# Performance work log

Hardware: AMD Instinct MI355X
Metric: run time of the kernel (lower is better)

## Reference

```python
import jax, jax.numpy as jnp
import numpy as np

BITS = 4
GROUP_SIZE = 128
IN_FEATURES = 4096
OUT_FEATURES = 11008
BATCH = 128


def setup_inputs() -> dict:
    key = jax.random.key(0)
    k1, k2, k3, k4 = jax.random.split(key, 4)
    x = jax.random.normal(k1, (BATCH, IN_FEATURES), dtype=jnp.float32)
    # packed 4-bit weights: each int32 holds 8 nibbles along the in-feature dim
    qweight = jax.random.randint(k2, (IN_FEATURES // 32 * BITS, OUT_FEATURES), 0, 2147483647, dtype=jnp.int32)
    n_groups = IN_FEATURES // GROUP_SIZE
    scales = jax.random.uniform(k3, (n_groups, OUT_FEATURES), dtype=jnp.float32) * 0.01 + 1e-3
    # note: in GPTQLinear_woo, `zeros` buffer already stores scale*zero_point
    zeros = jax.random.normal(k4, (n_groups, OUT_FEATURES), dtype=jnp.float32) * 0.01
    return {"x": x, "qweight": qweight, "scales": scales, "zeros": zeros}


def _dequant(qweight, scales, zeros):
    out_f = qweight.shape[1]
    shifts = jnp.arange(0, 32, BITS, dtype=jnp.int32)  # [8]
    # [in/8, 8, out] -> unpack nibbles (mask kills arithmetic-shift sign bits)
    w = (qweight[:, None, :] >> shifts[None, :, None]) & (2 ** BITS - 1)
    w = w.reshape(-1, GROUP_SIZE, out_f).astype(scales.dtype)  # [n_groups, gs, out]
    w = scales[:, None, :] * w - zeros[:, None, :]
    return w.reshape(-1, out_f)  # [in, out]


def reference(x, qweight, scales, zeros):
    w = _dequant(qweight, scales, zeros)
    return jnp.matmul(x, w)  # [batch, out]
```

## Files before the change

### kernel.cpp

```cpp
#include <hip/hip_runtime.h>
#include <hip/hip_bf16.h>
#include <stdint.h>


#define IN_F   4096
#define OUT_F  11008
#define BATCH  128
#define SPLIT  4
#define KSLICE (IN_F / SPLIT)
#define NCH    (KSLICE / 64)
#define NCHG   (IN_F / 64)
#define NBN    86
#define NBLK   (NBN * 2 * SPLIT)
#define MN     (BATCH * OUT_F)

typedef __attribute__((ext_vector_type(8)))  short short8;
typedef __attribute__((ext_vector_type(16))) float f32x16;

static __device__ __forceinline__ unsigned int f2bf_pack(float lo, float hi) {
  unsigned int a = __float_as_uint(lo);
  unsigned int b = __float_as_uint(hi);
  a += 0x7FFFu + ((a >> 16) & 1u);
  b += 0x7FFFu + ((b >> 16) & 1u);
  return (a >> 16) | (b & 0xFFFF0000u);
}

__global__ __launch_bounds__(256) void cvt_swz(const float* __restrict__ x,
                                               uint4* __restrict__ xs) {
  int t  = blockIdx.x * 256 + threadIdx.x;
  int m  = t >> 9;
  int k  = (t & 511) * 8;
  float4 u0 = *(const float4*)(x + (size_t)m * IN_F + k);
  float4 u1 = *(const float4*)(x + (size_t)m * IN_F + k + 4);
  uint4 o;
  o.x = f2bf_pack(u0.x, u0.y);
  o.y = f2bf_pack(u0.z, u0.w);
  o.z = f2bf_pack(u1.x, u1.y);
  o.w = f2bf_pack(u1.z, u1.w);
  int mt = m >> 5, lo32 = m & 31;
  int cg = k >> 6, ks = (k >> 4) & 3, hi = (k >> 3) & 1;
  size_t idx = (size_t)(((mt * NCHG + cg) * 4 + ks) << 6) + hi * 32 + lo32;
  xs[idx] = o;
}

__global__ __launch_bounds__(256) void zero_out(float* __restrict__ out) {
  int base = (blockIdx.x * 256 + threadIdx.x) * 16;
  float4 z = {0.f, 0.f, 0.f, 0.f};
#pragma unroll
  for (int j = 0; j < 4; ++j) *(float4*)(out + base + j * 4) = z;
}

__global__ __launch_bounds__(256) void reduce_kernel(const float* __restrict__ part,
                                                     float* __restrict__ out) {
  int base = (blockIdx.x * 256 + threadIdx.x) * 8;
  float4 s0 = {0.f, 0.f, 0.f, 0.f}, s1 = s0;
#pragma unroll
  for (int s = 0; s < SPLIT; ++s) {
    const float* p = part + (size_t)s * MN + base;
    float4 a = *(const float4*)(p);
    float4 b = *(const float4*)(p + 4);
    s0.x += a.x; s0.y += a.y; s0.z += a.z; s0.w += a.w;
    s1.x += b.x; s1.y += b.y; s1.z += b.z; s1.w += b.w;
  }
  *(float4*)(out + base)     = s0;
  *(float4*)(out + base + 4) = s1;
}

static __device__ __forceinline__ short8 deq8(unsigned int q, float s, float z) {
  float f[8];
#pragma unroll
  for (int j = 0; j < 8; ++j)
    f[j] = s * (float)((q >> (4 * j)) & 0xFu) - z;
  union { unsigned int u[4]; short8 s8; } r;
#pragma unroll
  for (int j = 0; j < 4; ++j)
    r.u[j] = f2bf_pack(f[2 * j], f[2 * j + 1]);
  return r.s8;
}

#define LOAD_Q(S, CC) do {                                                     \
    _Pragma("unroll")                                                          \
    for (int ks_ = 0; ks_ < 4; ++ks_)                                          \
      qP[S][ks_] = qlane[(size_t)((CC) * 8 + ks_ * 2) * OUT_F];                \
  } while (0)

__global__ __launch_bounds__(256) void gptq_gemm(
    const uint4* __restrict__ xs,
    const int* __restrict__ qweight,
    const float* __restrict__ scales,
    const float* __restrict__ zeros,
    float* __restrict__ outp,
    int atomic_mode) {
  const int tid  = threadIdx.x;
  const int lane = tid & 63;
  const int wid  = tid >> 6;
  const int hi   = lane >> 5;
  const int lo32 = lane & 31;

  const int nb = blockIdx.x % NBN;
  const int mb = (blockIdx.x / NBN) & 1;
  const int sl = blockIdx.x / (NBN * 2);

  const int ncol = nb * 128 + wid * 32 + lo32;
  const int m0   = mb * 64;

  float* dst = atomic_mode ? outp : outp + (size_t)sl * MN;

  float sreg[8], zreg[8];
#pragma unroll
  for (int g = 0; g < 8; ++g) {
    sreg[g] = scales[(size_t)(sl * 8 + g) * OUT_F + ncol];
    zreg[g] = zeros [(size_t)(sl * 8 + g) * OUT_F + ncol];
  }

  const int* qlane = qweight + (size_t)(sl * (KSLICE / 8) + hi) * OUT_F + ncol;
  const uint4* aB0 = xs + (size_t)(((mb * 2 + 0) * NCHG + sl * NCH) << 8) + lane;
  const uint4* aB1 = xs + (size_t)(((mb * 2 + 1) * NCHG + sl * NCH) << 8) + lane;

  unsigned int qP[3][4];
  LOAD_Q(0, 0);
  LOAD_Q(1, 1);
  LOAD_Q(2, 2);

  f32x16 acc[2] = {};

#pragma unroll
  for (int cc = 0; cc < NCH; ++cc) {
    uint4 aF[2][4];
#pragma unroll
    for (int ks = 0; ks < 4; ++ks) {
      aF[0][ks] = aB0[(size_t)(cc * 4 + ks) << 6];
      aF[1][ks] = aB1[(size_t)(cc * 4 + ks) << 6];
    }

    const float s = sreg[cc >> 1], z = zreg[cc >> 1];
    short8 bF[4];
#pragma unroll
    for (int ks = 0; ks < 4; ++ks)
      bF[ks] = deq8(qP[cc % 3][ks], s, z);

    if (cc + 3 < NCH) LOAD_Q(cc % 3, cc + 3);

#pragma unroll
    for (int ks = 0; ks < 4; ++ks) {
      union { uint4 u; short8 s8; } a0, a1;
      a0.u = aF[0][ks];
      a1.u = aF[1][ks];
      acc[0] = __builtin_amdgcn_mfma_f32_32x32x16_bf16(a0.s8, bF[ks], acc[0], 0, 0, 0);
      acc[1] = __builtin_amdgcn_mfma_f32_32x32x16_bf16(a1.s8, bF[ks], acc[1], 0, 0, 0);
    }
  }

#pragma unroll
  for (int rt = 0; rt < 2; ++rt) {
#pragma unroll
    for (int reg = 0; reg < 16; ++reg) {
      int row = m0 + rt * 32 + 4 * hi + (reg & 3) + 8 * (reg >> 2);
      if (atomic_mode) {
        atomicAdd(dst + (size_t)row * OUT_F + ncol, acc[rt][reg]);
      } else {
        dst[(size_t)row * OUT_F + ncol] = acc[rt][reg];
      }
    }
  }
}

extern "C" void kernel_launch(void* const* d_in, const int* in_sizes, int n_in,
                              void* d_out, int out_size, void* d_ws, size_t ws_size,
                              hipStream_t stream) {
  const float* x       = (const float*)d_in[0];
  const int*   qweight = (const int*)d_in[1];
  const float* scales  = (const float*)d_in[2];
  const float* zeros   = (const float*)d_in[3];
  float*       outp    = (float*)d_out;

  const size_t xs_bytes   = (size_t)BATCH * IN_F * sizeof(unsigned short);
  const size_t part_bytes = (size_t)SPLIT * MN * sizeof(float);
  int partials = (ws_size >= xs_bytes + part_bytes) ? 1 : 0;

  uint4* xs   = (uint4*)d_ws;
  float* part = (float*)((char*)d_ws + xs_bytes);

  cvt_swz<<<256, 256, 0, stream>>>(x, xs);

  if (partials) {
    gptq_gemm<<<NBLK, 256, 0, stream>>>(xs, qweight, scales, zeros, part, 0);
    reduce_kernel<<<688, 256, 0, stream>>>(part, outp);
  } else {
    zero_out<<<344, 256, 0, stream>>>(outp);
    gptq_gemm<<<NBLK, 256, 0, stream>>>(xs, qweight, scales, zeros, outp, 1);
  }
}
```

Baseline: 43.30 us.

## Dequantize via bf16 magic-number trick and apply scales/zeros algebraically post-MFMA

After: 74.06 us. 71.0% more time.

```diff
diff --git a/kernel.cpp b/kernel.cpp
--- a/kernel.cpp
+++ b/kernel.cpp
@@ -8,11 +8,12 @@
 #define BATCH  128
 #define SPLIT  4
 #define KSLICE (IN_F / SPLIT)
-#define NCH    (KSLICE / 64)
+#define KSC    (KSLICE / 64)
 #define NCHG   (IN_F / 64)
 #define NBN    86
 #define NBLK   (NBN * 2 * SPLIT)
 #define MN     (BATCH * OUT_F)
+#define NGRP   (IN_F / 128)
 
 typedef __attribute__((ext_vector_type(8)))  short short8;
 typedef __attribute__((ext_vector_type(16))) float f32x16;
@@ -25,8 +26,15 @@
   return (a >> 16) | (b & 0xFFFF0000u);
 }
 
+static __device__ __forceinline__ float bf16_round_f32(float v) {
+  unsigned int u = __float_as_uint(v);
+  u += 0x7FFFu + ((u >> 16) & 1u);
+  return __uint_as_float(u & 0xFFFF0000u);
+}
+
 __global__ __launch_bounds__(256) void cvt_swz(const float* __restrict__ x,
-                                               uint4* __restrict__ xs) {
+                                               uint4* __restrict__ xs,
+                                               float* __restrict__ rsum) {
   int t  = blockIdx.x * 256 + threadIdx.x;
   int m  = t >> 9;
   int k  = (t & 511) * 8;
@@ -41,6 +49,19 @@
   int cg = k >> 6, ks = (k >> 4) & 3, hi = (k >> 3) & 1;
   size_t idx = (size_t)(((mt * NCHG + cg) * 4 + ks) << 6) + hi * 32 + lo32;
   xs[idx] = o;
+
+  float s8 = bf16_round_f32(u0.x) + bf16_round_f32(u0.y) +
+             bf16_round_f32(u0.z) + bf16_round_f32(u0.w) +
+             bf16_round_f32(u1.x) + bf16_round_f32(u1.y) +
+             bf16_round_f32(u1.z) + bf16_round_f32(u1.w);
+  s8 += __shfl_xor(s8, 1, 16);
+  s8 += __shfl_xor(s8, 2, 16);
+  s8 += __shfl_xor(s8, 4, 16);
+  s8 += __shfl_xor(s8, 8, 16);
+  if ((t & 15) == 0) {
+    int g = (t & 511) >> 4;
+    rsum[m * NGRP + g] = s8;
+  }
 }
 
 __global__ __launch_bounds__(256) void zero_out(float* __restrict__ out) {
@@ -66,29 +87,35 @@
   *(float4*)(out + base + 4) = s1;
 }
 
-static __device__ __forceinline__ short8 deq8(unsigned int q, float s, float z) {
-  float f[8];
-#pragma unroll
-  for (int j = 0; j < 8; ++j)
-    f[j] = s * (float)((q >> (4 * j)) & 0xFu) - z;
+static __device__ __forceinline__ short8 deq8i(unsigned int q) {
   union { unsigned int u[4]; short8 s8; } r;
 #pragma unroll
   for (int j = 0; j < 4; ++j)
-    r.u[j] = f2bf_pack(f[2 * j], f[2 * j + 1]);
+    r.u[j] = 0x43004300u | ((q >> (8 * j)) & 0xFu) |
+             (((q >> (8 * j + 4)) & 0xFu) << 16);
   return r.s8;
 }
 
-#define LOAD_Q(S, CC) do {                                                     \
+#define LOAD_A(SET, CH) do {                                                   \
+    _Pragma("unroll")                                                          \
+    for (int ks_ = 0; ks_ < 4; ++ks_) {                                        \
+      aP[SET][0][ks_] = aB0[(size_t)(((CH) * 4 + ks_)) << 6];                  \
+      aP[SET][1][ks_] = aB1[(size_t)(((CH) * 4 + ks_)) << 6];                  \
+    }                                                                          \
+  } while (0)
+
+#define LOAD_Q(S, CH) do {                                                     \
     _Pragma("unroll")                                                          \
     for (int ks_ = 0; ks_ < 4; ++ks_)                                          \
-      qP[S][ks_] = qlane[(size_t)((CC) * 8 + ks_ * 2) * OUT_F];                \
+      qP[S][ks_] = qlane[(size_t)((CH) * 8 + ks_ * 2) * OUT_F];                \
   } while (0)
 
-__global__ __launch_bounds__(256) void gptq_gemm(
+__global__ __launch_bounds__(256, 2) void gptq_gemm(
     const uint4* __restrict__ xs,
     const int* __restrict__ qweight,
     const float* __restrict__ scales,
     const float* __restrict__ zeros,
+    const float* __restrict__ rsum,
     float* __restrict__ outp,
     int atomic_mode) {
   const int tid  = threadIdx.x;
@@ -106,60 +133,78 @@
 
   float* dst = atomic_mode ? outp : outp + (size_t)sl * MN;
 
-  float sreg[8], zreg[8];
-#pragma unroll
-  for (int g = 0; g < 8; ++g) {
+  float sreg[8];
+#pragma unroll
+  for (int g = 0; g < 8; ++g)
     sreg[g] = scales[(size_t)(sl * 8 + g) * OUT_F + ncol];
-    zreg[g] = zeros [(size_t)(sl * 8 + g) * OUT_F + ncol];
-  }
 
   const int* qlane = qweight + (size_t)(sl * (KSLICE / 8) + hi) * OUT_F + ncol;
-  const uint4* aB0 = xs + (size_t)(((mb * 2 + 0) * NCHG + sl * NCH) << 8) + lane;
-  const uint4* aB1 = xs + (size_t)(((mb * 2 + 1) * NCHG + sl * NCH) << 8) + lane;
-
+  const uint4* aB0 = xs + ((size_t)((mb * 2 + 0) * NCHG + sl * KSC) << 8) + lane;
+  const uint4* aB1 = xs + ((size_t)((mb * 2 + 1) * NCHG + sl * KSC) << 8) + lane;
+
+  uint4 aP[2][2][4];
   unsigned int qP[3][4];
+
+  LOAD_A(0, 0);
   LOAD_Q(0, 0);
   LOAD_Q(1, 1);
   LOAD_Q(2, 2);
 
-  f32x16 acc[2] = {};
-
-#pragma unroll
-  for (int cc = 0; cc < NCH; ++cc) {
-    uint4 aF[2][4];
-#pragma unroll
-    for (int ks = 0; ks < 4; ++ks) {
-      aF[0][ks] = aB0[(size_t)(cc * 4 + ks) << 6];
-      aF[1][ks] = aB1[(size_t)(cc * 4 + ks) << 6];
-    }
-
-    const float s = sreg[cc >> 1], z = zreg[cc >> 1];
+  f32x16 acc[2]  = {};
+  f32x16 accg[2] = {};
+
+#pragma unroll
+  for (int cc = 0; cc < KSC; ++cc) {
+    const int p = cc & 1;
+    if (cc + 1 < KSC) LOAD_A(p ^ 1, cc + 1);
+
     short8 bF[4];
 #pragma unroll
     for (int ks = 0; ks < 4; ++ks)
-      bF[ks] = deq8(qP[cc % 3][ks], s, z);
-
-    if (cc + 3 < NCH) LOAD_Q(cc % 3, cc + 3);
+      bF[ks] = deq8i(qP[cc % 3][ks]);
+
+    if (cc + 3 < KSC) LOAD_Q(cc % 3, cc + 3);
 
 #pragma unroll
     for (int ks = 0; ks < 4; ++ks) {
       union { uint4 u; short8 s8; } a0, a1;
-      a0.u = aF[0][ks];
-      a1.u = aF[1][ks];
-      acc[0] = __builtin_amdgcn_mfma_f32_32x32x16_bf16(a0.s8, bF[ks], acc[0], 0, 0, 0);
-      acc[1] = __builtin_amdgcn_mfma_f32_32x32x16_bf16(a1.s8, bF[ks], acc[1], 0, 0, 0);
+      a0.u = aP[p][0][ks];
+      a1.u = aP[p][1][ks];
+      accg[0] = __builtin_amdgcn_mfma_f32_32x32x16_bf16(a0.s8, bF[ks], accg[0], 0, 0, 0);
+      accg[1] = __builtin_amdgcn_mfma_f32_32x32x16_bf16(a1.s8, bF[ks], accg[1], 0, 0, 0);
     }
-  }
-
-#pragma unroll
-  for (int rt = 0; rt < 2; ++rt) {
+
+    if (cc & 1) {
+      const float s = sreg[cc >> 1];
+#pragma unroll
+      for (int j = 0; j < 16; ++j) {
+        acc[0][j] += s * accg[0][j];
+        acc[1][j] += s * accg[1][j];
+        accg[0][j] = 0.f;
+        accg[1][j] = 0.f;
+      }
+    }
+  }
+
+  float cg[8];
+#pragma unroll
+  for (int g = 0; g < 8; ++g)
+    cg[g] = 128.f * sreg[g] + zeros[(size_t)(sl * 8 + g) * OUT_F + ncol];
+
+#pragma unroll
+  for (int mi = 0; mi < 2; ++mi) {
 #pragma unroll
     for (int reg = 0; reg < 16; ++reg) {
-      int row = m0 + rt * 32 + 4 * hi + (reg & 3) + 8 * (reg >> 2);
+      int row = m0 + mi * 32 + 4 * hi + (reg & 3) + 8 * (reg >> 2);
+      const float4* rp = (const float4*)(rsum + (size_t)row * NGRP + sl * 8);
+      float4 r0 = rp[0], r1 = rp[1];
+      float corr = cg[0] * r0.x + cg[1] * r0.y + cg[2] * r0.z + cg[3] * r0.w +
+                   cg[4] * r1.x + cg[5] * r1.y + cg[6] * r1.z + cg[7] * r1.w;
+      float val = acc[mi][reg] - corr;
       if (atomic_mode) {
-        atomicAdd(dst + (size_t)row * OUT_F + ncol, acc[rt][reg]);
+        atomicAdd(dst + (size_t)row * OUT_F + ncol, val);
       } else {
-        dst[(size_t)row * OUT_F + ncol] = acc[rt][reg];
+        dst[(size_t)row * OUT_F + ncol] = val;
       }
     }
   }
@@ -175,19 +220,21 @@
   float*       outp    = (float*)d_out;
 
   const size_t xs_bytes   = (size_t)BATCH * IN_F * sizeof(unsigned short);
+  const size_t rs_bytes   = (size_t)BATCH * NGRP * sizeof(float);
   const size_t part_bytes = (size_t)SPLIT * MN * sizeof(float);
-  int partials = (ws_size >= xs_bytes + part_bytes) ? 1 : 0;
+  int partials = (ws_size >= xs_bytes + rs_bytes + part_bytes) ? 1 : 0;
 
   uint4* xs   = (uint4*)d_ws;
-  float* part = (float*)((char*)d_ws + xs_bytes);
-
-  cvt_swz<<<256, 256, 0, stream>>>(x, xs);
+  float* rsum = (float*)((char*)d_ws + xs_bytes);
+  float* part = (float*)((char*)d_ws + xs_bytes + rs_bytes);
+
+  cvt_swz<<<256, 256, 0, stream>>>(x, xs, rsum);
 
   if (partials) {
-    gptq_gemm<<<NBLK, 256, 0, stream>>>(xs, qweight, scales, zeros, part, 0);
+    gptq_gemm<<<NBLK, 256, 0, stream>>>(xs, qweight, scales, zeros, rsum, part, 0);
     reduce_kernel<<<688, 256, 0, stream>>>(part, outp);
   } else {
     zero_out<<<344, 256, 0, stream>>>(outp);
-    gptq_gemm<<<NBLK, 256, 0, stream>>>(xs, qweight, scales, zeros, outp, 1);
-  }
-}
+    gptq_gemm<<<NBLK, 256, 0, stream>>>(xs, qweight, scales, zeros, rsum, outp, 1);
+  }
+}
```

## Split each block's K-slice across two wave teams with LDS reduction

Applied to the files above, without the earlier changes.

After: 48.68 us. 12.4% more time.

```diff
diff --git a/kernel.cpp b/kernel.cpp
--- a/kernel.cpp
+++ b/kernel.cpp
@@ -8,7 +8,8 @@
 #define BATCH  128
 #define SPLIT  4
 #define KSLICE (IN_F / SPLIT)
-#define NCH    (KSLICE / 64)
+#define KSC    (KSLICE / 64)
+#define KST    (KSC / 2)
 #define NCHG   (IN_F / 64)
 #define NBN    86
 #define NBLK   (NBN * 2 * SPLIT)
@@ -84,38 +85,42 @@
       qP[S][ks_] = qlane[(size_t)((CC) * 8 + ks_ * 2) * OUT_F];                \
   } while (0)
 
-__global__ __launch_bounds__(256) void gptq_gemm(
+__global__ __launch_bounds__(512) void gptq_gemm(
     const uint4* __restrict__ xs,
     const int* __restrict__ qweight,
     const float* __restrict__ scales,
     const float* __restrict__ zeros,
     float* __restrict__ outp,
     int atomic_mode) {
-  const int tid  = threadIdx.x;
-  const int lane = tid & 63;
-  const int wid  = tid >> 6;
-  const int hi   = lane >> 5;
-  const int lo32 = lane & 31;
+  __shared__ float red[4][2][16][64];
+
+  const int tid    = threadIdx.x;
+  const int lane   = tid & 63;
+  const int wid    = tid >> 6;
+  const int team   = wid >> 2;
+  const int wlocal = wid & 3;
+  const int hi     = lane >> 5;
+  const int lo32   = lane & 31;
 
   const int nb = blockIdx.x % NBN;
   const int mb = (blockIdx.x / NBN) & 1;
   const int sl = blockIdx.x / (NBN * 2);
 
-  const int ncol = nb * 128 + wid * 32 + lo32;
+  const int ncol = nb * 128 + wlocal * 32 + lo32;
   const int m0   = mb * 64;
 
   float* dst = atomic_mode ? outp : outp + (size_t)sl * MN;
 
-  float sreg[8], zreg[8];
-#pragma unroll
-  for (int g = 0; g < 8; ++g) {
-    sreg[g] = scales[(size_t)(sl * 8 + g) * OUT_F + ncol];
-    zreg[g] = zeros [(size_t)(sl * 8 + g) * OUT_F + ncol];
-  }
-
-  const int* qlane = qweight + (size_t)(sl * (KSLICE / 8) + hi) * OUT_F + ncol;
-  const uint4* aB0 = xs + (size_t)(((mb * 2 + 0) * NCHG + sl * NCH) << 8) + lane;
-  const uint4* aB1 = xs + (size_t)(((mb * 2 + 1) * NCHG + sl * NCH) << 8) + lane;
+  float sreg[4], zreg[4];
+#pragma unroll
+  for (int g = 0; g < 4; ++g) {
+    sreg[g] = scales[(size_t)(sl * 8 + team * 4 + g) * OUT_F + ncol];
+    zreg[g] = zeros [(size_t)(sl * 8 + team * 4 + g) * OUT_F + ncol];
+  }
+
+  const int* qlane = qweight + (size_t)(sl * (KSLICE / 8) + team * 64 + hi) * OUT_F + ncol;
+  const uint4* aB0 = xs + ((size_t)((mb * 2 + 0) * NCHG + sl * KSC + team * KST) << 8) + lane;
+  const uint4* aB1 = xs + ((size_t)((mb * 2 + 1) * NCHG + sl * KSC + team * KST) << 8) + lane;
 
   unsigned int qP[3][4];
   LOAD_Q(0, 0);
@@ -125,7 +130,7 @@
   f32x16 acc[2] = {};
 
 #pragma unroll
-  for (int cc = 0; cc < NCH; ++cc) {
+  for (int cc = 0; cc < KST; ++cc) {
     uint4 aF[2][4];
 #pragma unroll
     for (int ks = 0; ks < 4; ++ks) {
@@ -139,7 +144,7 @@
     for (int ks = 0; ks < 4; ++ks)
       bF[ks] = deq8(qP[cc % 3][ks], s, z);
 
-    if (cc + 3 < NCH) LOAD_Q(cc % 3, cc + 3);
+    if (cc + 3 < KST) LOAD_Q(cc % 3, cc + 3);
 
 #pragma unroll
     for (int ks = 0; ks < 4; ++ks) {
@@ -151,15 +156,27 @@
     }
   }
 
-#pragma unroll
-  for (int rt = 0; rt < 2; ++rt) {
-#pragma unroll
-    for (int reg = 0; reg < 16; ++reg) {
-      int row = m0 + rt * 32 + 4 * hi + (reg & 3) + 8 * (reg >> 2);
-      if (atomic_mode) {
-        atomicAdd(dst + (size_t)row * OUT_F + ncol, acc[rt][reg]);
-      } else {
-        dst[(size_t)row * OUT_F + ncol] = acc[rt][reg];
+  if (team == 1) {
+#pragma unroll
+    for (int mi = 0; mi < 2; ++mi)
+#pragma unroll
+      for (int reg = 0; reg < 16; ++reg)
+        red[wlocal][mi][reg][lane] = acc[mi][reg];
+  }
+  __syncthreads();
+
+  if (team == 0) {
+#pragma unroll
+    for (int mi = 0; mi < 2; ++mi) {
+#pragma unroll
+      for (int reg = 0; reg < 16; ++reg) {
+        float val = acc[mi][reg] + red[wlocal][mi][reg][lane];
+        int row = m0 + mi * 32 + 4 * hi + (reg & 3) + 8 * (reg >> 2);
+        if (atomic_mode) {
+          atomicAdd(dst + (size_t)row * OUT_F + ncol, val);
+        } else {
+          dst[(size_t)row * OUT_F + ncol] = val;
+        }
       }
     }
   }
@@ -184,10 +201,10 @@
   cvt_swz<<<256, 256, 0, stream>>>(x, xs);
 
   if (partials) {
-    gptq_gemm<<<NBLK, 256, 0, stream>>>(xs, qweight, scales, zeros, part, 0);
+    gptq_gemm<<<NBLK, 512, 0, stream>>>(xs, qweight, scales, zeros, part, 0);
     reduce_kernel<<<688, 256, 0, stream>>>(part, outp);
   } else {
     zero_out<<<344, 256, 0, stream>>>(outp);
-    gptq_gemm<<<NBLK, 256, 0, stream>>>(xs, qweight, scales, zeros, outp, 1);
-  }
-}
+    gptq_gemm<<<NBLK, 512, 0, stream>>>(xs, qweight, scales, zeros, outp, 1);
+  }
+}
```
